# Kernel tuning notes

Hardware: AMD Instinct MI355X
Metric: run time of the kernel (lower is better)

## Reference

```python
import jax, jax.numpy as jnp
import numpy as np

SCALE = 10.0
DIM = 512
DIM_HEAD = 64
HEADS = DIM // DIM_HEAD
LN_EPS = 1e-05
L2_EPS = 1e-12


def l2norm(t, axis=1):
    # Faithful to source: default axis=1 (token axis for [b, n, h, d] tensors)
    denom = jnp.clip(jnp.linalg.norm(t, ord=2, axis=axis, keepdims=True), L2_EPS)
    return t / denom


def setup_inputs() -> dict:
    key = jax.random.key(0)
    k1, k2, k3 = jax.random.split(key, 3)
    B, H, W, C = 8, 32, 32, 512
    x = jax.random.normal(k1, (B, H, W, C), dtype=jnp.float32)
    ln_scale = jnp.ones((C,), dtype=jnp.float32)
    # 1x1 convs == channel matmuls; fan-in scaled init
    w_qkv = jax.random.normal(k2, (C, 3 * DIM), dtype=jnp.float32) / np.sqrt(C)
    w_out = jax.random.normal(k3, (DIM, C), dtype=jnp.float32) / np.sqrt(DIM)
    b_out = jnp.zeros((C,), dtype=jnp.float32)
    return {"x": x, "ln_scale": ln_scale, "w_qkv": w_qkv, "w_out": w_out, "b_out": b_out}


def reference(x, ln_scale, w_qkv, w_out, b_out):
    B, H, W, C = x.shape
    N = H * W
    # LayerNorm over channels (use_bias=False, use_scale=True)
    mean = jnp.mean(x, axis=-1, keepdims=True)
    var = jnp.mean(jnp.square(x - mean), axis=-1, keepdims=True)
    y = (x - mean) * jax.lax.rsqrt(var + LN_EPS) * ln_scale
    # 1x1 conv QKV projection (no bias)
    qkv = jnp.einsum('bhwc,cf->bhwf', y, w_qkv)  # [B,H,W,3*DIM]
    q, k, v = jnp.split(qkv, 3, axis=-1)
    # b x y (h d) -> b (x y) h d
    def to_tokens(t):
        return t.reshape(B, N, HEADS, DIM_HEAD)
    q, k, v = map(to_tokens, (q, k, v))
    # l2norm over axis=1 (token axis), faithful to source default
    q = l2norm(q)
    k = l2norm(k)
    sim = jnp.einsum('bihd,bjhd->bhij', q, k) * SCALE  # [B,heads,N,N]
    attn = jax.nn.softmax(sim, axis=-1)
    out = jnp.einsum('bhij,bjhd->bhid', attn, v)  # [B,heads,N,d]
    # b h (x y) d -> b x y (h d)
    out = out.transpose(0, 2, 1, 3).reshape(B, H, W, HEADS * DIM_HEAD)
    # 1x1 output conv (with bias)
    out = jnp.einsum('bhwf,fc->bhwc', out, w_out) + b_out
    return out
```

## Files before the change

kernel.cpp:

```cpp
#include <hip/hip_runtime.h>

typedef __bf16 bf16x8 __attribute__((ext_vector_type(8)));
typedef float f32x4 __attribute__((ext_vector_type(4)));

#define DEV static __device__ __forceinline__

DEV unsigned short f2bf(float f) {
    union { __bf16 h; unsigned short s; } c; c.h = (__bf16)f; return c.s;
}
DEV float bf2f(unsigned short h) {
    union { unsigned u; float f; } c; c.u = ((unsigned)h) << 16; return c.f;
}
DEV unsigned packbf2(float a, float b) {
    union { __bf16 h[2]; unsigned u; } c;
    c.h[0] = (__bf16)a; c.h[1] = (__bf16)b; return c.u;
}

DEV f32x4 mfma16(bf16x8 a, bf16x8 b, f32x4 c) {
    return __builtin_amdgcn_mfma_f32_16x16x32_bf16(a, b, c, 0, 0, 0);
}

#define GLOAD16(gp, lp)                                                        \
    __builtin_amdgcn_global_load_lds(                                          \
        (const __attribute__((address_space(1))) unsigned int*)(gp),           \
        (__attribute__((address_space(3))) unsigned int*)(lp), 16, 0, 0)

__global__ __launch_bounds__(256) void ln_conv_kernel(const float* __restrict__ x,
                                                      const float* __restrict__ lnsc,
                                                      unsigned short* __restrict__ y,
                                                      float* __restrict__ ssq,
                                                      const float* __restrict__ wqkv,
                                                      const float* __restrict__ wout,
                                                      unsigned short* __restrict__ wqkvt,
                                                      unsigned short* __restrict__ woutt) {
    const int t = threadIdx.x;
    if (blockIdx.x >= 2048) {
        __shared__ __bf16 tile[64][65];
        const int wblk = blockIdx.x - 2048;
        const float* src;
        unsigned short* dst;
        int ldsrc, k0, f0;
        if (wblk < 192) {
            src = wqkv; dst = wqkvt; ldsrc = 1536;
            k0 = (wblk / 24) * 64; f0 = (wblk % 24) * 64;
        } else {
            int w2 = wblk - 192;
            src = wout; dst = woutt; ldsrc = 512;
            k0 = (w2 >> 3) * 64; f0 = (w2 & 7) * 64;
        }
#pragma unroll
        for (int j = 0; j < 16; j++) {
            int idx = t + j * 256;
            int a = idx >> 6, b2 = idx & 63;
            tile[b2][a] = (__bf16)src[(size_t)(k0 + a) * ldsrc + f0 + b2];
        }
        __syncthreads();
#pragma unroll
        for (int j = 0; j < 16; j++) {
            int idx = t + j * 256;
            int fb = idx >> 6, kc = idx & 63;
            union { __bf16 h; unsigned short s; } cv;
            cv.h = tile[fb][kc];
            dst[(size_t)(f0 + fb) * 512 + k0 + kc] = cv.s;
        }
        return;
    }
    if (blockIdx.x < 32) ssq[(blockIdx.x << 8) | t] = 0.0f;
    const int token = blockIdx.x * 4 + (t >> 6);
    const int lane = t & 63;
    const float4* xp = (const float4*)(x + (size_t)token * 512 + lane * 8);
    float4 v0 = xp[0], v1 = xp[1];
    float s = v0.x + v0.y + v0.z + v0.w + v1.x + v1.y + v1.z + v1.w;
    float s2 = v0.x * v0.x + v0.y * v0.y + v0.z * v0.z + v0.w * v0.w +
               v1.x * v1.x + v1.y * v1.y + v1.z * v1.z + v1.w * v1.w;
#pragma unroll
    for (int off = 1; off < 64; off <<= 1) {
        s += __shfl_xor(s, off);
        s2 += __shfl_xor(s2, off);
    }
    const float mean = s * (1.0f / 512.0f);
    const float var = s2 * (1.0f / 512.0f) - mean * mean;
    const float rstd = rsqrtf(var + 1e-5f);
    const float4* sp = (const float4*)(lnsc + lane * 8);
    float4 sc0 = sp[0], sc1 = sp[1];
    union { __bf16 h[8]; uint4 v; } pk;
    pk.h[0] = (__bf16)((v0.x - mean) * rstd * sc0.x);
    pk.h[1] = (__bf16)((v0.y - mean) * rstd * sc0.y);
    pk.h[2] = (__bf16)((v0.z - mean) * rstd * sc0.z);
    pk.h[3] = (__bf16)((v0.w - mean) * rstd * sc0.w);
    pk.h[4] = (__bf16)((v1.x - mean) * rstd * sc1.x);
    pk.h[5] = (__bf16)((v1.y - mean) * rstd * sc1.y);
    pk.h[6] = (__bf16)((v1.z - mean) * rstd * sc1.z);
    pk.h[7] = (__bf16)((v1.w - mean) * rstd * sc1.w);
    *(uint4*)(y + (size_t)token * 512 + lane * 8) = pk.v;
}

template <int WM, int WN, int NCOLS, bool OUT_BF16, bool BIAS, bool SSQ, bool VT>
__global__ __launch_bounds__(256) void gemm_bt(const unsigned short* __restrict__ A,
                                               const unsigned short* __restrict__ Bt,
                                               void* __restrict__ Cout,
                                               const float* __restrict__ bias,
                                               float* __restrict__ ssq,
                                               unsigned short* __restrict__ vt,
                                               int M, int K) {
    constexpr int BM = 2 * WM, BN = 2 * WN;
    constexpr int ASZ = BM * 64 * 2, BSZ = BN * 64 * 2;
    constexpr int NLA = WM / 16, NLB = WN / 16;
    constexpr int DBUF = 2 * (ASZ + BSZ);
    constexpr int TTB = VT ? 128 * 136 * 2 : 0;
    constexpr int LDSB = DBUF > TTB ? DBUF : TTB;
    __shared__ __align__(16) char smem[LDSB];
    const int t = threadIdx.x;
    const int w = t >> 6, lane = t & 63;
    const int g = lane >> 4, l15 = lane & 15;
    const int wr = w >> 1, wc = w & 1;
    const int bR = blockIdx.y, bC = blockIdx.x;
    f32x4 acc[NLA][NLB] = {};
    const size_t ldb = (size_t)K * 2;
    const char* Ag = (const char*)A + (size_t)bR * BM * ldb;
    const char* Bg = (const char*)Bt + (size_t)bC * BN * ldb;

#define GSTAGE(buf, kt_)                                                            \
    {                                                                               \
        char* Ad = smem + (buf) * (ASZ + BSZ);                                      \
        char* Bd = Ad + ASZ;                                                        \
        _Pragma("unroll") for (int i = 0; i < NLA; i++) {                           \
            int o = i * 4096 + t * 16;                                              \
            int row = o >> 7, kb = (o & 127) ^ ((row & 7) << 4);                    \
            GLOAD16(Ag + (size_t)row * ldb + (size_t)(kt_) * 2 + kb, Ad + o);       \
        }                                                                           \
        _Pragma("unroll") for (int i = 0; i < NLB; i++) {                           \
            int o = i * 4096 + t * 16;                                              \
            int row = o >> 7, kb = (o & 127) ^ ((row & 7) << 4);                    \
            GLOAD16(Bg + (size_t)row * ldb + (size_t)(kt_) * 2 + kb, Bd + o);       \
        }                                                                           \
    }

    GSTAGE(0, 0)
    const int NT = K >> 6;
    for (int tt = 0; tt < NT; ++tt) {
        const int cur = tt & 1;
        if (tt + 1 < NT) {
            GSTAGE(cur ^ 1, (tt + 1) * 64)
            asm volatile("s_waitcnt vmcnt(%0)" ::"n"(NLA + NLB) : "memory");
        } else {
            asm volatile("s_waitcnt vmcnt(0)" ::: "memory");
        }
        __builtin_amdgcn_s_barrier();
        const char* Ab = smem + cur * (ASZ + BSZ);
        const char* Bb = Ab + ASZ;
#pragma unroll
        for (int kk = 0; kk < 64; kk += 32) {
            bf16x8 a[NLA], bb[NLB];
#pragma unroll
            for (int m = 0; m < NLA; m++) {
                int row = wr * WM + m * 16 + l15;
                int kb = ((kk + g * 8) * 2) ^ ((row & 7) << 4);
                a[m] = *(const bf16x8*)(Ab + row * 128 + kb);
            }
#pragma unroll
            for (int n = 0; n < NLB; n++) {
                int row = wc * WN + n * 16 + l15;
                int kb = ((kk + g * 8) * 2) ^ ((row & 7) << 4);
                bb[n] = *(const bf16x8*)(Bb + row * 128 + kb);
            }
#pragma unroll
            for (int m = 0; m < NLA; m++)
#pragma unroll
                for (int n = 0; n < NLB; n++)
                    acc[m][n] = mfma16(a[m], bb[n], acc[m][n]);
        }
        __builtin_amdgcn_s_barrier();
    }
#undef GSTAGE

    const int rbase = bR * BM + wr * WM;
    const int cbase = bC * BN + wc * WN;
    if (!VT || bC < 8) {
#pragma unroll
        for (int m = 0; m < NLA; m++)
#pragma unroll
            for (int n = 0; n < NLB; n++)
#pragma unroll
                for (int r = 0; r < 4; r++) {
                    int row = rbase + m * 16 + g * 4 + r;
                    int col = cbase + n * 16 + l15;
                    float v = acc[m][n][r];
                    if constexpr (OUT_BF16)
                        ((unsigned short*)Cout)[(size_t)row * NCOLS + col] = f2bf(v);
                    else
                        ((float*)Cout)[(size_t)row * NCOLS + col] =
                            v + (BIAS ? bias[col] : 0.f);
                }
    }
    if constexpr (SSQ) {
        if (bC < 8) {
            const int bb2 = bR >> 3;
#pragma unroll
            for (int n = 0; n < NLB; n++) {
                float ps = 0.f;
#pragma unroll
                for (int m = 0; m < NLA; m++)
#pragma unroll
                    for (int r = 0; r < 4; r++) ps += acc[m][n][r] * acc[m][n][r];
                ps += __shfl_xor(ps, 16);
                ps += __shfl_xor(ps, 32);
                if (g == 0)
                    atomicAdd(&ssq[bb2 * 1024 + cbase + n * 16 + l15], ps);
            }
        }
    }
    if constexpr (VT) {
        if (bC >= 8) {
            unsigned short* TT = (unsigned short*)smem;
            __syncthreads();
#pragma unroll
            for (int m = 0; m < NLA; m++)
#pragma unroll
                for (int n = 0; n < NLB; n++)
#pragma unroll
                    for (int r = 0; r < 4; r++) {
                        int row = wr * WM + m * 16 + g * 4 + r;
                        int col = wc * WN + n * 16 + l15;
                        TT[col * 136 + row] = f2bf(acc[m][n][r]);
                    }
            __syncthreads();
            const int f = t >> 1, th = t & 1;
            const int fh = (bC - 8) * 128 + f;
            const int hh = fh >> 6, dd = fh & 63;
            const int bb3 = bR >> 3, nb = (bR & 7) * 128;
            unsigned short* dst =
                vt + (((size_t)bb3 * 8 + hh) * 64 + dd) * 1024 + nb + th * 64;
            const unsigned short* srcp = TT + f * 136 + th * 64;
#pragma unroll
            for (int j = 0; j < 8; j++)
                *(uint4*)(dst + j * 8) = *(const uint4*)(srcp + j * 8);
        }
    }
}

__global__ __launch_bounds__(256) void attn_kernel(const unsigned short* __restrict__ qkv,
                                                   const unsigned short* __restrict__ vt,
                                                   unsigned short* __restrict__ attnout,
                                                   const float* __restrict__ ssq) {
    __shared__ unsigned short Ks[2][4096];
    __shared__ unsigned short Vs[2][4096];
    __shared__ unsigned short Ps[4][2048];
    __shared__ float smq[64];
    const int t = threadIdx.x, w = t >> 6, lane = t & 63;
    const int g = lane >> 4, l15 = lane & 15;
    const int qt = blockIdx.x, bh = blockIdx.y;
    const int b = bh >> 3, h = bh & 7;
    const size_t qrow0 = (size_t)b * 1024 + qt * 128;
    const char* qg = (const char*)qkv;
    const char* vg = (const char*)vt;

    if (t < 64) {
        float nq = fmaxf(sqrtf(ssq[b * 1024 + h * 64 + t]), 1e-12f);
        float nk = fmaxf(sqrtf(ssq[b * 1024 + 512 + h * 64 + t]), 1e-12f);
        smq[t] = 14.42695040888963f / (nq * nk);
    }
    __syncthreads();

    bf16x8 qf[2][2];
#pragma unroll
    for (int qb = 0; qb < 2; qb++)
#pragma unroll
        for (int c = 0; c < 2; c++) {
            union { bf16x8 v; unsigned short u[8]; } in, ov;
            in.v = *(const bf16x8*)(qkv + (qrow0 + w * 32 + qb * 16 + l15) * 1536 +
                                    h * 64 + c * 32 + g * 8);
#pragma unroll
            for (int j = 0; j < 8; j++)
                ov.u[j] = f2bf(bf2f(in.u[j]) * smq[c * 32 + g * 8 + j]);
            qf[qb][c] = ov.v;
        }

    f32x4 accO[2][4] = {};
    float prs[2] = {0.f, 0.f};

#define ASTAGE(buf, tt_)                                                              \
    {                                                                                 \
        const int kt_ = (tt_) * 64;                                                   \
        _Pragma("unroll") for (int i = 0; i < 2; i++) {                               \
            int o = i * 4096 + t * 16;                                                \
            int row = o >> 7, kb = (o & 127) ^ ((row & 7) << 4);                      \
            GLOAD16(qg + ((size_t)b * 1024 + kt_ + row) * 3072 + 1024 + h * 128 + kb, \
                    (char*)Ks[buf] + o);                                              \
            GLOAD16(vg + ((size_t)bh * 64 + row) * 2048 + (size_t)kt_ * 2 + kb,       \
                    (char*)Vs[buf] + o);                                              \
        }                                                                             \
    }

    ASTAGE(0, 0)
    for (int tt = 0; tt < 16; ++tt) {
        const int cur = tt & 1;
        if (tt < 15) {
            ASTAGE(cur ^ 1, tt + 1)
            asm volatile("s_waitcnt vmcnt(4)" ::: "memory");
        } else {
            asm volatile("s_waitcnt vmcnt(0)" ::: "memory");
        }
        __builtin_amdgcn_s_barrier();

        f32x4 s[2][4] = {};
        __builtin_amdgcn_s_setprio(1);
#pragma unroll
        for (int c = 0; c < 2; c++) {
            bf16x8 bk[4];
#pragma unroll
            for (int n = 0; n < 4; n++) {
                int krow = n * 16 + l15;
                int kb = ((c * 32 + g * 8) * 2) ^ ((krow & 7) << 4);
                bk[n] = *(const bf16x8*)((const char*)Ks[cur] + krow * 128 + kb);
            }
#pragma unroll
            for (int qb = 0; qb < 2; qb++)
#pragma unroll
                for (int n = 0; n < 4; n++)
                    s[qb][n] = mfma16(bk[n], qf[qb][c], s[qb][n]);
        }
        __builtin_amdgcn_s_setprio(0);
#pragma unroll
        for (int qb = 0; qb < 2; qb++) {
            const int prow = qb * 16 + l15;
#pragma unroll
            for (int n = 0; n < 4; n++) {
                float p0 = __builtin_amdgcn_exp2f(s[qb][n][0]);
                float p1 = __builtin_amdgcn_exp2f(s[qb][n][1]);
                float p2 = __builtin_amdgcn_exp2f(s[qb][n][2]);
                float p3 = __builtin_amdgcn_exp2f(s[qb][n][3]);
                prs[qb] += (p0 + p1) + (p2 + p3);
                uint2 pk;
                pk.x = packbf2(p0, p1);
                pk.y = packbf2(p2, p3);
                int kb = ((n * 16 + g * 4) * 2) ^ ((prow & 7) << 4);
                *(uint2*)((char*)Ps[w] + prow * 128 + kb) = pk;
            }
        }
        __builtin_amdgcn_s_setprio(1);
#pragma unroll
        for (int c2 = 0; c2 < 2; c2++) {
            bf16x8 bv[4];
#pragma unroll
            for (int n = 0; n < 4; n++) {
                int vrow = n * 16 + l15;
                int kb = ((c2 * 32 + g * 8) * 2) ^ ((vrow & 7) << 4);
                bv[n] = *(const bf16x8*)((const char*)Vs[cur] + vrow * 128 + kb);
            }
#pragma unroll
            for (int qb = 0; qb < 2; qb++) {
                const int prow = qb * 16 + l15;
                int kb = ((c2 * 32 + g * 8) * 2) ^ ((prow & 7) << 4);
                bf16x8 ap = *(const bf16x8*)((const char*)Ps[w] + prow * 128 + kb);
#pragma unroll
                for (int n = 0; n < 4; n++)
                    accO[qb][n] = mfma16(ap, bv[n], accO[qb][n]);
            }
        }
        __builtin_amdgcn_s_setprio(0);
        __builtin_amdgcn_s_barrier();
    }
#undef ASTAGE
#pragma unroll
    for (int qb = 0; qb < 2; qb++) {
        float tot = prs[qb];
        tot += __shfl_xor(tot, 16);
        tot += __shfl_xor(tot, 32);
        float inv[4];
#pragma unroll
        for (int r = 0; r < 4; r++) inv[r] = 1.0f / __shfl(tot, g * 4 + r);
#pragma unroll
        for (int n = 0; n < 4; n++)
#pragma unroll
            for (int r = 0; r < 4; r++)
                attnout[(qrow0 + w * 32 + qb * 16 + g * 4 + r) * 512 + h * 64 + n * 16 +
                        l15] = f2bf(accO[qb][n][r] * inv[r]);
    }
}

extern "C" void kernel_launch(void* const* d_in, const int* in_sizes, int n_in,
                              void* d_out, int out_size, void* d_ws, size_t ws_size,
                              hipStream_t stream) {
    const float* x = (const float*)d_in[0];
    const float* ln_scale = (const float*)d_in[1];
    const float* w_qkv = (const float*)d_in[2];
    const float* w_out = (const float*)d_in[3];
    const float* b_out = (const float*)d_in[4];
    float* out = (float*)d_out;

    char* ws = (char*)d_ws;
    unsigned short* y = (unsigned short*)(ws + 0);
    unsigned short* wqkvt = (unsigned short*)(ws + 8388608);
    unsigned short* woutt = (unsigned short*)(ws + 9961472);
    unsigned short* qkv = (unsigned short*)(ws + 10485760);
    unsigned short* vt = (unsigned short*)(ws + 35651584);
    float* ssq = (float*)(ws + 44040192);
    unsigned short* attnout = (unsigned short*)(ws + 0);

    ln_conv_kernel<<<2304, 256, 0, stream>>>(x, ln_scale, y, ssq, w_qkv, w_out, wqkvt,
                                             woutt);
    gemm_bt<64, 64, 1536, true, false, true, true><<<dim3(12, 64), 256, 0, stream>>>(
        y, wqkvt, qkv, nullptr, ssq, vt, 8192, 512);
    attn_kernel<<<dim3(8, 64), 256, 0, stream>>>(qkv, vt, attnout, ssq);
    gemm_bt<32, 64, 512, false, true, false, false><<<dim3(4, 128), 256, 0, stream>>>(
        attnout, woutt, out, b_out, nullptr, nullptr, 8192, 512);
}
```

Baseline: 78.22 us.

## Deepen attention K/V prefetch to four buffers, single-buffer QKV GEMM

The attention kernel now keeps four K/V LDS buffers and processes two key tiles per barrier pair, prefetching the next two tiles ahead. This halves the number of barriers and deepens the memory pipeline. The QKV projection GEMM gets a new single-buffer path that loads and computes with full syncs each step, cutting LDS use so more blocks can fit per CU. The output GEMM keeps double buffering. The larger attention LDS footprint may lower occupancy there, and the single-buffer GEMM loses load/compute overlap.

```diff
diff --git a/kernel.cpp b/kernel.cpp
--- a/kernel.cpp
+++ b/kernel.cpp
@@ -95,7 +95,8 @@
     *(uint4*)(y + (size_t)token * 512 + lane * 8) = pk.v;
 }
 
-template <int WM, int WN, int NCOLS, bool OUT_BF16, bool BIAS, bool SSQ, bool VT>
+template <int WM, int WN, int NCOLS, bool OUT_BF16, bool BIAS, bool SSQ, bool VT,
+          bool DB>
 __global__ __launch_bounds__(256) void gemm_bt(const unsigned short* __restrict__ A,
                                                const unsigned short* __restrict__ Bt,
                                                void* __restrict__ Cout,
@@ -106,9 +107,10 @@
     constexpr int BM = 2 * WM, BN = 2 * WN;
     constexpr int ASZ = BM * 64 * 2, BSZ = BN * 64 * 2;
     constexpr int NLA = WM / 16, NLB = WN / 16;
-    constexpr int DBUF = 2 * (ASZ + BSZ);
+    constexpr int NBUF = DB ? 2 : 1;
+    constexpr int STG = NBUF * (ASZ + BSZ);
     constexpr int TTB = VT ? 128 * 136 * 2 : 0;
-    constexpr int LDSB = DBUF > TTB ? DBUF : TTB;
+    constexpr int LDSB = STG > TTB ? STG : TTB;
     __shared__ __align__(16) char smem[LDSB];
     const int t = threadIdx.x;
     const int w = t >> 6, lane = t & 63;
@@ -136,43 +138,54 @@
         }                                                                           \
     }
 
-    GSTAGE(0, 0)
+#define GCOMPUTE(buf)                                                               \
+    {                                                                               \
+        const char* Ab = smem + (buf) * (ASZ + BSZ);                                \
+        const char* Bb = Ab + ASZ;                                                  \
+        _Pragma("unroll") for (int kk = 0; kk < 64; kk += 32) {                     \
+            bf16x8 a[NLA], bb[NLB];                                                 \
+            _Pragma("unroll") for (int m = 0; m < NLA; m++) {                       \
+                int row = wr * WM + m * 16 + l15;                                   \
+                int kb = ((kk + g * 8) * 2) ^ ((row & 7) << 4);                     \
+                a[m] = *(const bf16x8*)(Ab + row * 128 + kb);                       \
+            }                                                                       \
+            _Pragma("unroll") for (int n = 0; n < NLB; n++) {                       \
+                int row = wc * WN + n * 16 + l15;                                   \
+                int kb = ((kk + g * 8) * 2) ^ ((row & 7) << 4);                     \
+                bb[n] = *(const bf16x8*)(Bb + row * 128 + kb);                      \
+            }                                                                       \
+            _Pragma("unroll") for (int m = 0; m < NLA; m++)                         \
+                _Pragma("unroll") for (int n = 0; n < NLB; n++)                     \
+                    acc[m][n] = mfma16(a[m], bb[n], acc[m][n]);                     \
+        }                                                                           \
+    }
+
     const int NT = K >> 6;
-    for (int tt = 0; tt < NT; ++tt) {
-        const int cur = tt & 1;
-        if (tt + 1 < NT) {
-            GSTAGE(cur ^ 1, (tt + 1) * 64)
-            asm volatile("s_waitcnt vmcnt(%0)" ::"n"(NLA + NLB) : "memory");
-        } else {
+    if constexpr (DB) {
+        GSTAGE(0, 0)
+        for (int tt = 0; tt < NT; ++tt) {
+            const int cur = tt & 1;
+            if (tt + 1 < NT) {
+                GSTAGE(cur ^ 1, (tt + 1) * 64)
+                asm volatile("s_waitcnt vmcnt(%0)" ::"n"(NLA + NLB) : "memory");
+            } else {
+                asm volatile("s_waitcnt vmcnt(0)" ::: "memory");
+            }
+            __builtin_amdgcn_s_barrier();
+            GCOMPUTE(cur)
+            __builtin_amdgcn_s_barrier();
+        }
+    } else {
+        for (int tt = 0; tt < NT; ++tt) {
+            __syncthreads();
+            GSTAGE(0, tt * 64)
             asm volatile("s_waitcnt vmcnt(0)" ::: "memory");
-        }
-        __builtin_amdgcn_s_barrier();
-        const char* Ab = smem + cur * (ASZ + BSZ);
-        const char* Bb = Ab + ASZ;
-#pragma unroll
-        for (int kk = 0; kk < 64; kk += 32) {
-            bf16x8 a[NLA], bb[NLB];
-#pragma unroll
-            for (int m = 0; m < NLA; m++) {
-                int row = wr * WM + m * 16 + l15;
-                int kb = ((kk + g * 8) * 2) ^ ((row & 7) << 4);
-                a[m] = *(const bf16x8*)(Ab + row * 128 + kb);
-            }
-#pragma unroll
-            for (int n = 0; n < NLB; n++) {
-                int row = wc * WN + n * 16 + l15;
-                int kb = ((kk + g * 8) * 2) ^ ((row & 7) << 4);
-                bb[n] = *(const bf16x8*)(Bb + row * 128 + kb);
-            }
-#pragma unroll
-            for (int m = 0; m < NLA; m++)
-#pragma unroll
-                for (int n = 0; n < NLB; n++)
-                    acc[m][n] = mfma16(a[m], bb[n], acc[m][n]);
-        }
-        __builtin_amdgcn_s_barrier();
+            __syncthreads();
+            GCOMPUTE(0)
+        }
     }
 #undef GSTAGE
+#undef GCOMPUTE
 
     const int rbase = bR * BM + wr * WM;
     const int cbase = bC * BN + wc * WN;
@@ -243,8 +256,8 @@
                                                    const unsigned short* __restrict__ vt,
                                                    unsigned short* __restrict__ attnout,
                                                    const float* __restrict__ ssq) {
-    __shared__ unsigned short Ks[2][4096];
-    __shared__ unsigned short Vs[2][4096];
+    __shared__ unsigned short Ks[4][4096];
+    __shared__ unsigned short Vs[4][4096];
     __shared__ unsigned short Ps[4][2048];
     __shared__ float smq[64];
     const int t = threadIdx.x, w = t >> 6, lane = t & 63;
@@ -292,17 +305,7 @@
         }                                                                             \
     }
 
-    ASTAGE(0, 0)
-    for (int tt = 0; tt < 16; ++tt) {
-        const int cur = tt & 1;
-        if (tt < 15) {
-            ASTAGE(cur ^ 1, tt + 1)
-            asm volatile("s_waitcnt vmcnt(4)" ::: "memory");
-        } else {
-            asm volatile("s_waitcnt vmcnt(0)" ::: "memory");
-        }
-        __builtin_amdgcn_s_barrier();
-
+    auto tile_compute = [&](int buf) {
         f32x4 s[2][4] = {};
         __builtin_amdgcn_s_setprio(1);
 #pragma unroll
@@ -312,7 +315,7 @@
             for (int n = 0; n < 4; n++) {
                 int krow = n * 16 + l15;
                 int kb = ((c * 32 + g * 8) * 2) ^ ((krow & 7) << 4);
-                bk[n] = *(const bf16x8*)((const char*)Ks[cur] + krow * 128 + kb);
+                bk[n] = *(const bf16x8*)((const char*)Ks[buf] + krow * 128 + kb);
             }
 #pragma unroll
             for (int qb = 0; qb < 2; qb++)
@@ -346,7 +349,7 @@
             for (int n = 0; n < 4; n++) {
                 int vrow = n * 16 + l15;
                 int kb = ((c2 * 32 + g * 8) * 2) ^ ((vrow & 7) << 4);
-                bv[n] = *(const bf16x8*)((const char*)Vs[cur] + vrow * 128 + kb);
+                bv[n] = *(const bf16x8*)((const char*)Vs[buf] + vrow * 128 + kb);
             }
 #pragma unroll
             for (int qb = 0; qb < 2; qb++) {
@@ -359,6 +362,22 @@
             }
         }
         __builtin_amdgcn_s_setprio(0);
+    };
+
+    ASTAGE(0, 0)
+    ASTAGE(1, 1)
+    for (int pt = 0; pt < 8; ++pt) {
+        const int b0 = (2 * pt) & 3, b1 = (2 * pt + 1) & 3;
+        if (pt < 7) {
+            ASTAGE((2 * pt + 2) & 3, 2 * pt + 2)
+            ASTAGE((2 * pt + 3) & 3, 2 * pt + 3)
+            asm volatile("s_waitcnt vmcnt(8)" ::: "memory");
+        } else {
+            asm volatile("s_waitcnt vmcnt(0)" ::: "memory");
+        }
+        __builtin_amdgcn_s_barrier();
+        tile_compute(b0);
+        tile_compute(b1);
         __builtin_amdgcn_s_barrier();
     }
 #undef ASTAGE
@@ -400,9 +419,10 @@
 
     ln_conv_kernel<<<2304, 256, 0, stream>>>(x, ln_scale, y, ssq, w_qkv, w_out, wqkvt,
                                              woutt);
-    gemm_bt<64, 64, 1536, true, false, true, true><<<dim3(12, 64), 256, 0, stream>>>(
-        y, wqkvt, qkv, nullptr, ssq, vt, 8192, 512);
+    gemm_bt<64, 64, 1536, true, false, true, true, false>
+        <<<dim3(12, 64), 256, 0, stream>>>(y, wqkvt, qkv, nullptr, ssq, vt, 8192, 512);
     attn_kernel<<<dim3(8, 64), 256, 0, stream>>>(qkv, vt, attnout, ssq);
-    gemm_bt<32, 64, 512, false, true, false, false><<<dim3(4, 128), 256, 0, stream>>>(
-        attnout, woutt, out, b_out, nullptr, nullptr, 8192, 512);
-}
+    gemm_bt<32, 64, 512, false, true, false, false, true>
+        <<<dim3(4, 128), 256, 0, stream>>>(attnout, woutt, out, b_out, nullptr, nullptr,
+                                           8192, 512);
+}
```

Measured after the change: 86.84 us. 1.11x slower.
